# Optimization experiments

Measured on AMD Instinct MI355X. Metric: run time of the kernel, lower is better.

## Reference

```python
import jax, jax.numpy as jnp
import numpy as np

NUM_USERS = 100000
NUM_ITEMS = 100000
EMBED_DIM = 64
BATCH = 4096
MAX_NEIGH = 50


def setup_inputs() -> dict:
    key = jax.random.key(0)
    ks = jax.random.split(key, 12)
    d = EMBED_DIM
    nodes = jax.random.randint(ks[0], (BATCH,), 0, NUM_USERS)
    neighbors = jax.random.randint(ks[1], (BATCH, MAX_NEIGH), 0, NUM_ITEMS)
    lengths = 1 + jax.random.randint(ks[2], (BATCH,), 0, MAX_NEIGH)  # ragged sizes in [1, MAX_NEIGH]
    u_table = jax.random.normal(ks[3], (NUM_USERS, d), dtype=jnp.float32) * 0.1
    i_table = jax.random.normal(ks[4], (NUM_ITEMS, d), dtype=jnp.float32) * 0.1
    # GraphRec-style attention MLP: Linear(2d,d) -> relu -> Linear(d,d) -> relu -> Linear(d,1) -> softmax
    W1 = jax.random.normal(ks[5], (2 * d, d), dtype=jnp.float32) * (1.0 / np.sqrt(2 * d))
    b1 = jnp.zeros((d,), dtype=jnp.float32)
    W2 = jax.random.normal(ks[6], (d, d), dtype=jnp.float32) * (1.0 / np.sqrt(d))
    b2 = jnp.zeros((d,), dtype=jnp.float32)
    W3 = jax.random.normal(ks[7], (d, 1), dtype=jnp.float32) * (1.0 / np.sqrt(d))
    b3 = jnp.zeros((1,), dtype=jnp.float32)
    return {"u_table": u_table, "i_table": i_table, "W1": W1, "b1": b1,
            "W2": W2, "b2": b2, "W3": W3, "b3": b3,
            "nodes": nodes, "neighbors": neighbors, "lengths": lengths}


def reference(u_table, i_table, W1, b1, W2, b2, W3, b3, nodes, neighbors, lengths):
    # is_user=True: gather item features for neighbors, user feature for the node itself.
    neighs = i_table[neighbors]            # [B, L, d]
    node = u_table[nodes]                  # [B, d]
    B, L, d = neighs.shape
    x = jnp.concatenate([neighs, jnp.broadcast_to(node[:, None, :], (B, L, d))], axis=-1)  # [B, L, 2d]
    h = jax.nn.relu(x @ W1 + b1)           # [B, L, d]
    h = jax.nn.relu(h @ W2 + b2)           # [B, L, d]
    logits = (h @ W3 + b3)[..., 0]         # [B, L]
    mask = jnp.arange(L)[None, :] < lengths[:, None]  # ragged neighbor mask
    logits = jnp.where(mask, logits, -jnp.inf)
    att = jax.nn.softmax(logits, axis=1)   # softmax over each node's neighbors (dim=0 per-node in torch)
    # embedding = (neighs^T att)^T  ==  sum_l att[b,l] * neighs[b,l,:]
    return jnp.einsum("bl,bld->bd", att, neighs)  # [B, d]
```

## Files before the change

### kernel.cpp

```cpp
#include <hip/hip_runtime.h>
#include <math.h>

#define LMAX  50
#define NWAVE 2048

typedef short bf16x8 __attribute__((ext_vector_type(8)));
typedef float f32x4  __attribute__((ext_vector_type(4)));
union bfu { bf16x8 v; unsigned u[4]; };

__device__ __forceinline__ unsigned cvt_pk(float lo, float hi) {
    unsigned r;
    asm("v_cvt_pk_bf16_f32 %0, %1, %2" : "=v"(r) : "v"(lo), "v"(hi));
    return r;
}
__device__ __forceinline__ bf16x8 cvt8f(float4 a, float4 b) {
    bfu r;
    r.u[0] = cvt_pk(a.x, a.y); r.u[1] = cvt_pk(a.z, a.w);
    r.u[2] = cvt_pk(b.x, b.y); r.u[3] = cvt_pk(b.z, b.w);
    return r.v;
}
__device__ __forceinline__ float bf2f(short s) {
    union { unsigned u; float f; } v; v.u = ((unsigned)(unsigned short)s) << 16;
    return v.f;
}

__device__ __forceinline__ void process_elem(
    const float* __restrict__ i_table, float* __restrict__ out,
    int b, int len, const int (&idx)[6],
    bf16x8 axu0, bf16x8 axu1,
    const bf16x8 (&w1f)[4][4], const bf16x8 (&w2f)[2][4],
    const float (&b1v)[4], const f32x4 (&b2r)[4], const f32x4 (&w3r)[4],
    unsigned short* __restrict__ hw,
    int l15, int g)
{
    const int g8    = g * 8;
    const int ntile = (len + 15) >> 4;

    float4 LA[2][4];
    #define ISSUE_T(t) if ((t) < ntile) { \
        const float* xp = i_table + (size_t)idx[t] * 64 + g8; \
        LA[(t) & 1][0] = *(const float4*)(xp); \
        LA[(t) & 1][1] = *(const float4*)(xp + 4); \
        LA[(t) & 1][2] = *(const float4*)(xp + 32); \
        LA[(t) & 1][3] = *(const float4*)(xp + 36); \
    }
    ISSUE_T(0)
    ISSUE_T(1)

    f32x4 hn[4];
    #pragma unroll
    for (int nt = 0; nt < 4; ++nt)
        hn[nt] = (f32x4){b1v[nt], b1v[nt], b1v[nt], b1v[nt]};
    #pragma unroll
    for (int nt = 0; nt < 4; ++nt)
        hn[nt] = __builtin_amdgcn_mfma_f32_16x16x32_bf16(axu0, w1f[2][nt], hn[nt], 0, 0, 0);
    #pragma unroll
    for (int nt = 0; nt < 4; ++nt)
        hn[nt] = __builtin_amdgcn_mfma_f32_16x16x32_bf16(axu1, w1f[3][nt], hn[nt], 0, 0, 0);

    float m = -INFINITY, ssum = 0.f;
    float accW[16];
    #pragma unroll
    for (int i = 0; i < 16; ++i) accW[i] = 0.f;

    #pragma unroll
    for (int t = 0; t < 4; ++t) {
        if (t < ntile) {
            bf16x8 a0 = cvt8f(LA[t & 1][0], LA[t & 1][1]);
            bf16x8 a1 = cvt8f(LA[t & 1][2], LA[t & 1][3]);
            if (t + 2 < 4) ISSUE_T(t + 2)

            f32x4 acc[4];
            #pragma unroll
            for (int nt = 0; nt < 4; ++nt) acc[nt] = hn[nt];
            #pragma unroll
            for (int nt = 0; nt < 4; ++nt)
                acc[nt] = __builtin_amdgcn_mfma_f32_16x16x32_bf16(a0, w1f[0][nt], acc[nt], 0, 0, 0);
            #pragma unroll
            for (int nt = 0; nt < 4; ++nt)
                acc[nt] = __builtin_amdgcn_mfma_f32_16x16x32_bf16(a1, w1f[1][nt], acc[nt], 0, 0, 0);

            #pragma unroll
            for (int nt = 0; nt < 4; ++nt) {
                unsigned p0 = cvt_pk(fmaxf(acc[nt][0], 0.f), fmaxf(acc[nt][1], 0.f));
                unsigned p1 = cvt_pk(fmaxf(acc[nt][2], 0.f), fmaxf(acc[nt][3], 0.f));
                hw[(g * 4 + 0) * 72 + nt * 16 + l15] = (unsigned short)p0;
                hw[(g * 4 + 1) * 72 + nt * 16 + l15] = (unsigned short)(p0 >> 16);
                hw[(g * 4 + 2) * 72 + nt * 16 + l15] = (unsigned short)p1;
                hw[(g * 4 + 3) * 72 + nt * 16 + l15] = (unsigned short)(p1 >> 16);
            }
            bf16x8 h0 = *(const bf16x8*)&hw[l15 * 72 + g8];
            bf16x8 h1 = *(const bf16x8*)&hw[l15 * 72 + 32 + g8];

            f32x4 c2[4];
            #pragma unroll
            for (int nt = 0; nt < 4; ++nt) c2[nt] = b2r[nt];
            #pragma unroll
            for (int nt = 0; nt < 4; ++nt)
                c2[nt] = __builtin_amdgcn_mfma_f32_16x16x32_bf16(w2f[0][nt], h0, c2[nt], 0, 0, 0);
            #pragma unroll
            for (int nt = 0; nt < 4; ++nt)
                c2[nt] = __builtin_amdgcn_mfma_f32_16x16x32_bf16(w2f[1][nt], h1, c2[nt], 0, 0, 0);

            float ls = 0.f;
            #pragma unroll
            for (int nt = 0; nt < 4; ++nt) {
                ls = fmaf(fmaxf(c2[nt][0], 0.f), w3r[nt][0], ls);
                ls = fmaf(fmaxf(c2[nt][1], 0.f), w3r[nt][1], ls);
                ls = fmaf(fmaxf(c2[nt][2], 0.f), w3r[nt][2], ls);
                ls = fmaf(fmaxf(c2[nt][3], 0.f), w3r[nt][3], ls);
            }
            ls += __shfl_xor(ls, 16);
            ls += __shfl_xor(ls, 32);

            const int rabs = t * 16 + l15;
            const float lgv = (rabs < len) ? ls : -INFINITY;

            float tm = fmaxf(lgv, __shfl_xor(lgv, 1));
            tm = fmaxf(tm, __shfl_xor(tm, 2));
            tm = fmaxf(tm, __shfl_xor(tm, 4));
            tm = fmaxf(tm, __shfl_xor(tm, 8));
            if (tm > m) {
                const float sc = __expf(m - tm);
                ssum *= sc;
                #pragma unroll
                for (int i = 0; i < 16; ++i) accW[i] *= sc;
                m = tm;
            }
            const float er = __expf(lgv - m);
            ssum += er;

            #pragma unroll
            for (int i = 0; i < 8; ++i) {
                accW[i]     = fmaf(er, bf2f(a0[i]), accW[i]);
                accW[8 + i] = fmaf(er, bf2f(a1[i]), accW[8 + i]);
            }
        }
    }
    #undef ISSUE_T

    #pragma unroll
    for (int i = 0; i < 16; ++i) {
        accW[i] += __shfl_xor(accW[i], 1);
        accW[i] += __shfl_xor(accW[i], 2);
        accW[i] += __shfl_xor(accW[i], 4);
        accW[i] += __shfl_xor(accW[i], 8);
    }
    float ss = ssum;
    ss += __shfl_xor(ss, 1);
    ss += __shfl_xor(ss, 2);
    ss += __shfl_xor(ss, 4);
    ss += __shfl_xor(ss, 8);
    const float inv = 1.f / ss;
    if (l15 == 0) {
        float4 o0 = make_float4(accW[0]  * inv, accW[1]  * inv, accW[2]  * inv, accW[3]  * inv);
        float4 o1 = make_float4(accW[4]  * inv, accW[5]  * inv, accW[6]  * inv, accW[7]  * inv);
        float4 o2 = make_float4(accW[8]  * inv, accW[9]  * inv, accW[10] * inv, accW[11] * inv);
        float4 o3 = make_float4(accW[12] * inv, accW[13] * inv, accW[14] * inv, accW[15] * inv);
        *(float4*)(out + b * 64 +      g8)     = o0;
        *(float4*)(out + b * 64 +      g8 + 4) = o1;
        *(float4*)(out + b * 64 + 32 + g8)     = o2;
        *(float4*)(out + b * 64 + 32 + g8 + 4) = o3;
    }
}

__global__ __launch_bounds__(256, 2) void graphrec_k(
    const float* __restrict__ u_table, const float* __restrict__ i_table,
    const float* __restrict__ W1, const float* __restrict__ b1,
    const float* __restrict__ W2, const float* __restrict__ b2,
    const float* __restrict__ W3, const float* __restrict__ b3,
    const int* __restrict__ nodes, const int* __restrict__ neighbors,
    const int* __restrict__ lengths, float* __restrict__ out)
{
    __shared__ __attribute__((aligned(16))) short WL[24][64][8];
    __shared__ __attribute__((aligned(16))) unsigned short Hs[4][16 * 72];

    const int tid  = threadIdx.x;
    const int w    = tid >> 6, lane = tid & 63;
    const int l15  = lane & 15, g = lane >> 4, g8 = g * 8;

    for (int f = w; f < 24; f += 4) {
        const float* Ws = (f < 16) ? W1 : W2;
        const int    fi = (f < 16) ? f : f - 16;
        const int    ks = fi >> 2, nt = fi & 3;
        const float* p  = Ws + (ks * 32 + g8) * 64 + nt * 16 + l15;
        bfu r;
        r.u[0] = cvt_pk(p[0 * 64], p[1 * 64]);
        r.u[1] = cvt_pk(p[2 * 64], p[3 * 64]);
        r.u[2] = cvt_pk(p[4 * 64], p[5 * 64]);
        r.u[3] = cvt_pk(p[6 * 64], p[7 * 64]);
        *(bf16x8*)&WL[f][lane][0] = r.v;
    }
    __syncthreads();

    bf16x8 w1f[4][4], w2f[2][4];
    #pragma unroll
    for (int ks = 0; ks < 4; ++ks)
        #pragma unroll
        for (int nt = 0; nt < 4; ++nt)
            w1f[ks][nt] = *(const bf16x8*)&WL[ks * 4 + nt][lane][0];
    #pragma unroll
    for (int ks = 0; ks < 2; ++ks)
        #pragma unroll
        for (int nt = 0; nt < 4; ++nt)
            w2f[ks][nt] = *(const bf16x8*)&WL[16 + ks * 4 + nt][lane][0];

    float b1v[4];
    f32x4 b2r[4], w3r[4];
    #pragma unroll
    for (int nt = 0; nt < 4; ++nt) {
        b1v[nt] = b1[nt * 16 + l15];
        b2r[nt] = *(const f32x4*)(b2 + nt * 16 + 4 * g);
        w3r[nt] = *(const f32x4*)(W3 + nt * 16 + 4 * g);
    }

    const int wid = blockIdx.x * 4 + w;
    const int b0  = wid, b1e = wid + NWAVE;

    const int len0 = lengths[b0], len1 = lengths[b1e];
    const int nd0  = nodes[b0],   nd1  = nodes[b1e];

    int idx0[6] = {0, 0, 0, 0, 0, 0}, idx1[6] = {0, 0, 0, 0, 0, 0};
    const int nt0 = (len0 + 15) >> 4, nt1 = (len1 + 15) >> 4;
    #pragma unroll
    for (int t = 0; t < 4; ++t) {
        int r = t * 16 + l15; if (r >= len0) r = len0 - 1;
        if (t < nt0) idx0[t] = neighbors[b0 * LMAX + r];
    }
    #pragma unroll
    for (int t = 0; t < 4; ++t) {
        int r = t * 16 + l15; if (r >= len1) r = len1 - 1;
        if (t < nt1) idx1[t] = neighbors[b1e * LMAX + r];
    }

    const float* up0 = u_table + (size_t)nd0 * 64 + g8;
    const float* up1 = u_table + (size_t)nd1 * 64 + g8;
    float4 U00 = *(const float4*)(up0);
    float4 U01 = *(const float4*)(up0 + 4);
    float4 U02 = *(const float4*)(up0 + 32);
    float4 U03 = *(const float4*)(up0 + 36);
    float4 U10 = *(const float4*)(up1);
    float4 U11 = *(const float4*)(up1 + 4);
    float4 U12 = *(const float4*)(up1 + 32);
    float4 U13 = *(const float4*)(up1 + 36);

    process_elem(i_table, out, b0, len0, idx0,
                 cvt8f(U00, U01), cvt8f(U02, U03),
                 w1f, w2f, b1v, b2r, w3r, &Hs[w][0], l15, g);

    process_elem(i_table, out, b1e, len1, idx1,
                 cvt8f(U10, U11), cvt8f(U12, U13),
                 w1f, w2f, b1v, b2r, w3r, &Hs[w][0], l15, g);
}

extern "C" void kernel_launch(void* const* d_in, const int* in_sizes, int n_in,
                              void* d_out, int out_size, void* d_ws, size_t ws_size,
                              hipStream_t stream) {
    const float* u_table   = (const float*)d_in[0];
    const float* i_table   = (const float*)d_in[1];
    const float* W1        = (const float*)d_in[2];
    const float* b1        = (const float*)d_in[3];
    const float* W2        = (const float*)d_in[4];
    const float* b2        = (const float*)d_in[5];
    const float* W3        = (const float*)d_in[6];
    const float* b3        = (const float*)d_in[7];
    const int*   nodes     = (const int*)d_in[8];
    const int*   neighbors = (const int*)d_in[9];
    const int*   lengths   = (const int*)d_in[10];
    float* out = (float*)d_out;

    graphrec_k<<<dim3(NWAVE / 4), dim3(256), 0, stream>>>(
        u_table, i_table, W1, b1, W2, b2, W3, b3, nodes, neighbors, lengths, out);
}
```

Baseline: 22.41 us.

## Prefetch all neighbor tiles for both batch elements and hoist index loads before weight staging

Moves the lengths, nodes, neighbor index and user-row loads ahead of the shared-memory weight conversion so their latency overlaps with that setup. Instead of a two-deep rolling prefetch per element, all four neighbor tiles of the first element are issued up front, and the second element's tiles are issued interleaved with the first element's compute. This deepens memory-level parallelism for the random gathers but holds 32 float4 registers of staged data per lane, which raises register pressure and may hurt occupancy or cause spills under the 2-block launch bound.

```diff
diff --git a/kernel.cpp b/kernel.cpp
--- a/kernel.cpp
+++ b/kernel.cpp
@@ -24,121 +24,86 @@
     return v.f;
 }
 
-__device__ __forceinline__ void process_elem(
-    const float* __restrict__ i_table, float* __restrict__ out,
-    int b, int len, const int (&idx)[6],
-    bf16x8 axu0, bf16x8 axu1,
+__device__ __forceinline__ void tile_compute(
+    int t, int len, bf16x8 a0, bf16x8 a1,
+    const f32x4 (&hn)[4],
     const bf16x8 (&w1f)[4][4], const bf16x8 (&w2f)[2][4],
-    const float (&b1v)[4], const f32x4 (&b2r)[4], const f32x4 (&w3r)[4],
-    unsigned short* __restrict__ hw,
-    int l15, int g)
+    const f32x4 (&b2r)[4], const f32x4 (&w3r)[4],
+    unsigned short* __restrict__ hw, int l15, int g,
+    float& m, float& ssum, float (&accW)[16])
 {
-    const int g8    = g * 8;
-    const int ntile = (len + 15) >> 4;
-
-    float4 LA[2][4];
-    #define ISSUE_T(t) if ((t) < ntile) { \
-        const float* xp = i_table + (size_t)idx[t] * 64 + g8; \
-        LA[(t) & 1][0] = *(const float4*)(xp); \
-        LA[(t) & 1][1] = *(const float4*)(xp + 4); \
-        LA[(t) & 1][2] = *(const float4*)(xp + 32); \
-        LA[(t) & 1][3] = *(const float4*)(xp + 36); \
-    }
-    ISSUE_T(0)
-    ISSUE_T(1)
-
-    f32x4 hn[4];
-    #pragma unroll
-    for (int nt = 0; nt < 4; ++nt)
-        hn[nt] = (f32x4){b1v[nt], b1v[nt], b1v[nt], b1v[nt]};
-    #pragma unroll
-    for (int nt = 0; nt < 4; ++nt)
-        hn[nt] = __builtin_amdgcn_mfma_f32_16x16x32_bf16(axu0, w1f[2][nt], hn[nt], 0, 0, 0);
-    #pragma unroll
-    for (int nt = 0; nt < 4; ++nt)
-        hn[nt] = __builtin_amdgcn_mfma_f32_16x16x32_bf16(axu1, w1f[3][nt], hn[nt], 0, 0, 0);
-
-    float m = -INFINITY, ssum = 0.f;
-    float accW[16];
-    #pragma unroll
-    for (int i = 0; i < 16; ++i) accW[i] = 0.f;
-
-    #pragma unroll
-    for (int t = 0; t < 4; ++t) {
-        if (t < ntile) {
-            bf16x8 a0 = cvt8f(LA[t & 1][0], LA[t & 1][1]);
-            bf16x8 a1 = cvt8f(LA[t & 1][2], LA[t & 1][3]);
-            if (t + 2 < 4) ISSUE_T(t + 2)
-
-            f32x4 acc[4];
-            #pragma unroll
-            for (int nt = 0; nt < 4; ++nt) acc[nt] = hn[nt];
-            #pragma unroll
-            for (int nt = 0; nt < 4; ++nt)
-                acc[nt] = __builtin_amdgcn_mfma_f32_16x16x32_bf16(a0, w1f[0][nt], acc[nt], 0, 0, 0);
-            #pragma unroll
-            for (int nt = 0; nt < 4; ++nt)
-                acc[nt] = __builtin_amdgcn_mfma_f32_16x16x32_bf16(a1, w1f[1][nt], acc[nt], 0, 0, 0);
-
-            #pragma unroll
-            for (int nt = 0; nt < 4; ++nt) {
-                unsigned p0 = cvt_pk(fmaxf(acc[nt][0], 0.f), fmaxf(acc[nt][1], 0.f));
-                unsigned p1 = cvt_pk(fmaxf(acc[nt][2], 0.f), fmaxf(acc[nt][3], 0.f));
-                hw[(g * 4 + 0) * 72 + nt * 16 + l15] = (unsigned short)p0;
-                hw[(g * 4 + 1) * 72 + nt * 16 + l15] = (unsigned short)(p0 >> 16);
-                hw[(g * 4 + 2) * 72 + nt * 16 + l15] = (unsigned short)p1;
-                hw[(g * 4 + 3) * 72 + nt * 16 + l15] = (unsigned short)(p1 >> 16);
-            }
-            bf16x8 h0 = *(const bf16x8*)&hw[l15 * 72 + g8];
-            bf16x8 h1 = *(const bf16x8*)&hw[l15 * 72 + 32 + g8];
-
-            f32x4 c2[4];
-            #pragma unroll
-            for (int nt = 0; nt < 4; ++nt) c2[nt] = b2r[nt];
-            #pragma unroll
-            for (int nt = 0; nt < 4; ++nt)
-                c2[nt] = __builtin_amdgcn_mfma_f32_16x16x32_bf16(w2f[0][nt], h0, c2[nt], 0, 0, 0);
-            #pragma unroll
-            for (int nt = 0; nt < 4; ++nt)
-                c2[nt] = __builtin_amdgcn_mfma_f32_16x16x32_bf16(w2f[1][nt], h1, c2[nt], 0, 0, 0);
-
-            float ls = 0.f;
-            #pragma unroll
-            for (int nt = 0; nt < 4; ++nt) {
-                ls = fmaf(fmaxf(c2[nt][0], 0.f), w3r[nt][0], ls);
-                ls = fmaf(fmaxf(c2[nt][1], 0.f), w3r[nt][1], ls);
-                ls = fmaf(fmaxf(c2[nt][2], 0.f), w3r[nt][2], ls);
-                ls = fmaf(fmaxf(c2[nt][3], 0.f), w3r[nt][3], ls);
-            }
-            ls += __shfl_xor(ls, 16);
-            ls += __shfl_xor(ls, 32);
-
-            const int rabs = t * 16 + l15;
-            const float lgv = (rabs < len) ? ls : -INFINITY;
-
-            float tm = fmaxf(lgv, __shfl_xor(lgv, 1));
-            tm = fmaxf(tm, __shfl_xor(tm, 2));
-            tm = fmaxf(tm, __shfl_xor(tm, 4));
-            tm = fmaxf(tm, __shfl_xor(tm, 8));
-            if (tm > m) {
-                const float sc = __expf(m - tm);
-                ssum *= sc;
-                #pragma unroll
-                for (int i = 0; i < 16; ++i) accW[i] *= sc;
-                m = tm;
-            }
-            const float er = __expf(lgv - m);
-            ssum += er;
-
-            #pragma unroll
-            for (int i = 0; i < 8; ++i) {
-                accW[i]     = fmaf(er, bf2f(a0[i]), accW[i]);
-                accW[8 + i] = fmaf(er, bf2f(a1[i]), accW[8 + i]);
-            }
-        }
-    }
-    #undef ISSUE_T
-
+    const int g8 = g * 8;
+
+    f32x4 acc[4];
+    #pragma unroll
+    for (int nt = 0; nt < 4; ++nt) acc[nt] = hn[nt];
+    #pragma unroll
+    for (int nt = 0; nt < 4; ++nt)
+        acc[nt] = __builtin_amdgcn_mfma_f32_16x16x32_bf16(a0, w1f[0][nt], acc[nt], 0, 0, 0);
+    #pragma unroll
+    for (int nt = 0; nt < 4; ++nt)
+        acc[nt] = __builtin_amdgcn_mfma_f32_16x16x32_bf16(a1, w1f[1][nt], acc[nt], 0, 0, 0);
+
+    #pragma unroll
+    for (int nt = 0; nt < 4; ++nt) {
+        unsigned p0 = cvt_pk(fmaxf(acc[nt][0], 0.f), fmaxf(acc[nt][1], 0.f));
+        unsigned p1 = cvt_pk(fmaxf(acc[nt][2], 0.f), fmaxf(acc[nt][3], 0.f));
+        hw[(g * 4 + 0) * 72 + nt * 16 + l15] = (unsigned short)p0;
+        hw[(g * 4 + 1) * 72 + nt * 16 + l15] = (unsigned short)(p0 >> 16);
+        hw[(g * 4 + 2) * 72 + nt * 16 + l15] = (unsigned short)p1;
+        hw[(g * 4 + 3) * 72 + nt * 16 + l15] = (unsigned short)(p1 >> 16);
+    }
+    bf16x8 h0 = *(const bf16x8*)&hw[l15 * 72 + g8];
+    bf16x8 h1 = *(const bf16x8*)&hw[l15 * 72 + 32 + g8];
+
+    f32x4 c2[4];
+    #pragma unroll
+    for (int nt = 0; nt < 4; ++nt) c2[nt] = b2r[nt];
+    #pragma unroll
+    for (int nt = 0; nt < 4; ++nt)
+        c2[nt] = __builtin_amdgcn_mfma_f32_16x16x32_bf16(w2f[0][nt], h0, c2[nt], 0, 0, 0);
+    #pragma unroll
+    for (int nt = 0; nt < 4; ++nt)
+        c2[nt] = __builtin_amdgcn_mfma_f32_16x16x32_bf16(w2f[1][nt], h1, c2[nt], 0, 0, 0);
+
+    float ls = 0.f;
+    #pragma unroll
+    for (int nt = 0; nt < 4; ++nt) {
+        ls = fmaf(fmaxf(c2[nt][0], 0.f), w3r[nt][0], ls);
+        ls = fmaf(fmaxf(c2[nt][1], 0.f), w3r[nt][1], ls);
+        ls = fmaf(fmaxf(c2[nt][2], 0.f), w3r[nt][2], ls);
+        ls = fmaf(fmaxf(c2[nt][3], 0.f), w3r[nt][3], ls);
+    }
+    ls += __shfl_xor(ls, 16);
+    ls += __shfl_xor(ls, 32);
+
+    const int rabs = t * 16 + l15;
+    const float lgv = (rabs < len) ? ls : -INFINITY;
+
+    float tm = fmaxf(lgv, __shfl_xor(lgv, 1));
+    tm = fmaxf(tm, __shfl_xor(tm, 2));
+    tm = fmaxf(tm, __shfl_xor(tm, 4));
+    tm = fmaxf(tm, __shfl_xor(tm, 8));
+    if (tm > m) {
+        const float sc = __expf(m - tm);
+        ssum *= sc;
+        #pragma unroll
+        for (int i = 0; i < 16; ++i) accW[i] *= sc;
+        m = tm;
+    }
+    const float er = __expf(lgv - m);
+    ssum += er;
+    #pragma unroll
+    for (int i = 0; i < 8; ++i) {
+        accW[i]     = fmaf(er, bf2f(a0[i]), accW[i]);
+        accW[8 + i] = fmaf(er, bf2f(a1[i]), accW[8 + i]);
+    }
+}
+
+__device__ __forceinline__ void finalize_elem(
+    float (&accW)[16], float ssum, float* __restrict__ out,
+    int b, int l15, int g)
+{
     #pragma unroll
     for (int i = 0; i < 16; ++i) {
         accW[i] += __shfl_xor(accW[i], 1);
@@ -152,6 +117,7 @@
     ss += __shfl_xor(ss, 4);
     ss += __shfl_xor(ss, 8);
     const float inv = 1.f / ss;
+    const int g8 = g * 8;
     if (l15 == 0) {
         float4 o0 = make_float4(accW[0]  * inv, accW[1]  * inv, accW[2]  * inv, accW[3]  * inv);
         float4 o1 = make_float4(accW[4]  * inv, accW[5]  * inv, accW[6]  * inv, accW[7]  * inv);
@@ -178,6 +144,31 @@
     const int tid  = threadIdx.x;
     const int w    = tid >> 6, lane = tid & 63;
     const int l15  = lane & 15, g = lane >> 4, g8 = g * 8;
+
+    const int wid = blockIdx.x * 4 + w;
+    const int b0  = wid, b1e = wid + NWAVE;
+    const int len0 = lengths[b0], len1 = lengths[b1e];
+    const int nd0  = nodes[b0],   nd1  = nodes[b1e];
+    const int nt0  = (len0 + 15) >> 4, nt1 = (len1 + 15) >> 4;
+
+    int idx0[4], idx1[4];
+    #pragma unroll
+    for (int t = 0; t < 4; ++t) {
+        int r0 = t * 16 + l15; if (r0 >= len0) r0 = len0 - 1;
+        idx0[t] = (t < nt0) ? neighbors[b0 * LMAX + r0] : 0;
+        int r1 = t * 16 + l15; if (r1 >= len1) r1 = len1 - 1;
+        idx1[t] = (t < nt1) ? neighbors[b1e * LMAX + r1] : 0;
+    }
+    const float* up0 = u_table + (size_t)nd0 * 64 + g8;
+    const float* up1 = u_table + (size_t)nd1 * 64 + g8;
+    float4 U00 = *(const float4*)(up0);
+    float4 U01 = *(const float4*)(up0 + 4);
+    float4 U02 = *(const float4*)(up0 + 32);
+    float4 U03 = *(const float4*)(up0 + 36);
+    float4 U10 = *(const float4*)(up1);
+    float4 U11 = *(const float4*)(up1 + 4);
+    float4 U12 = *(const float4*)(up1 + 32);
+    float4 U13 = *(const float4*)(up1 + 36);
 
     for (int f = w; f < 24; f += 4) {
         const float* Ws = (f < 16) ? W1 : W2;
@@ -214,52 +205,94 @@
         w3r[nt] = *(const f32x4*)(W3 + nt * 16 + 4 * g);
     }
 
-    const int wid = blockIdx.x * 4 + w;
-    const int b0  = wid, b1e = wid + NWAVE;
-
-    const int len0 = lengths[b0], len1 = lengths[b1e];
-    const int nd0  = nodes[b0],   nd1  = nodes[b1e];
-
-    int idx0[6] = {0, 0, 0, 0, 0, 0}, idx1[6] = {0, 0, 0, 0, 0, 0};
-    const int nt0 = (len0 + 15) >> 4, nt1 = (len1 + 15) >> 4;
+    float4 LA0[4][4], LA1[4][4];
+    #define ISSUE0(t) if ((t) < nt0) { \
+        const float* xp = i_table + (size_t)idx0[t] * 64 + g8; \
+        LA0[t][0] = *(const float4*)(xp); \
+        LA0[t][1] = *(const float4*)(xp + 4); \
+        LA0[t][2] = *(const float4*)(xp + 32); \
+        LA0[t][3] = *(const float4*)(xp + 36); \
+    }
+    #define ISSUE1(t) if ((t) < nt1) { \
+        const float* xp = i_table + (size_t)idx1[t] * 64 + g8; \
+        LA1[t][0] = *(const float4*)(xp); \
+        LA1[t][1] = *(const float4*)(xp + 4); \
+        LA1[t][2] = *(const float4*)(xp + 32); \
+        LA1[t][3] = *(const float4*)(xp + 36); \
+    }
+    ISSUE0(0) ISSUE0(1) ISSUE0(2) ISSUE0(3)
+
+    bf16x8 ax0 = cvt8f(U00, U01), ax1 = cvt8f(U02, U03);
+    f32x4 hn0[4];
+    #pragma unroll
+    for (int nt = 0; nt < 4; ++nt)
+        hn0[nt] = (f32x4){b1v[nt], b1v[nt], b1v[nt], b1v[nt]};
+    #pragma unroll
+    for (int nt = 0; nt < 4; ++nt)
+        hn0[nt] = __builtin_amdgcn_mfma_f32_16x16x32_bf16(ax0, w1f[2][nt], hn0[nt], 0, 0, 0);
+    #pragma unroll
+    for (int nt = 0; nt < 4; ++nt)
+        hn0[nt] = __builtin_amdgcn_mfma_f32_16x16x32_bf16(ax1, w1f[3][nt], hn0[nt], 0, 0, 0);
+
+    unsigned short* hw = &Hs[w][0];
+
+    float m0 = -INFINITY, ss0 = 0.f;
+    float accW0[16];
+    #pragma unroll
+    for (int i = 0; i < 16; ++i) accW0[i] = 0.f;
+
     #pragma unroll
     for (int t = 0; t < 4; ++t) {
-        int r = t * 16 + l15; if (r >= len0) r = len0 - 1;
-        if (t < nt0) idx0[t] = neighbors[b0 * LMAX + r];
-    }
+        if (t < nt0) {
+            bf16x8 a0 = cvt8f(LA0[t][0], LA0[t][1]);
+            bf16x8 a1 = cvt8f(LA0[t][2], LA0[t][3]);
+            ISSUE1(t)
+            tile_compute(t, len0, a0, a1, hn0, w1f, w2f, b2r, w3r,
+                         hw, l15, g, m0, ss0, accW0);
+        } else {
+            ISSUE1(t)
+        }
+    }
+    finalize_elem(accW0, ss0, out, b0, l15, g);
+
+    bf16x8 bx0 = cvt8f(U10, U11), bx1 = cvt8f(U12, U13);
+    f32x4 hn1[4];
+    #pragma unroll
+    for (int nt = 0; nt < 4; ++nt)
+        hn1[nt] = (f32x4){b1v[nt], b1v[nt], b1v[nt], b1v[nt]};
+    #pragma unroll
+    for (int nt = 0; nt < 4; ++nt)
+        hn1[nt] = __builtin_amdgcn_mfma_f32_16x16x32_bf16(bx0, w1f[2][nt], hn1[nt], 0, 0, 0);
+    #pragma unroll
+    for (int nt = 0; nt < 4; ++nt)
+        hn1[nt] = __builtin_amdgcn_mfma_f32_16x16x32_bf16(bx1, w1f[3][nt], hn1[nt], 0, 0, 0);
+
+    float m1 = -INFINITY, ss1 = 0.f;
+    float accW1[16];
+    #pragma unroll
+    for (int i = 0; i < 16; ++i) accW1[i] = 0.f;
+
     #pragma unroll
     for (int t = 0; t < 4; ++t) {
-        int r = t * 16 + l15; if (r >= len1) r = len1 - 1;
-        if (t < nt1) idx1[t] = neighbors[b1e * LMAX + r];
-    }
-
-    const float* up0 = u_table + (size_t)nd0 * 64 + g8;
-    const float* up1 = u_table + (size_t)nd1 * 64 + g8;
-    float4 U00 = *(const float4*)(up0);
-    float4 U01 = *(const float4*)(up0 + 4);
-    float4 U02 = *(const float4*)(up0 + 32);
-    float4 U03 = *(const float4*)(up0 + 36);
-    float4 U10 = *(const float4*)(up1);
-    float4 U11 = *(const float4*)(up1 + 4);
-    float4 U12 = *(const float4*)(up1 + 32);
-    float4 U13 = *(const float4*)(up1 + 36);
-
-    process_elem(i_table, out, b0, len0, idx0,
-                 cvt8f(U00, U01), cvt8f(U02, U03),
-                 w1f, w2f, b1v, b2r, w3r, &Hs[w][0], l15, g);
-
-    process_elem(i_table, out, b1e, len1, idx1,
-                 cvt8f(U10, U11), cvt8f(U12, U13),
-                 w1f, w2f, b1v, b2r, w3r, &Hs[w][0], l15, g);
+        if (t < nt1) {
+            bf16x8 a0 = cvt8f(LA1[t][0], LA1[t][1]);
+            bf16x8 a1 = cvt8f(LA1[t][2], LA1[t][3]);
+            tile_compute(t, len1, a0, a1, hn1, w1f, w2f, b2r, w3r,
+                         hw, l15, g, m1, ss1, accW1);
+        }
+    }
+    finalize_elem(accW1, ss1, out, b1e, l15, g);
+    #undef ISSUE0
+    #undef ISSUE1
 }
 
 extern "C" void kernel_launch(void* const* d_in, const int* in_sizes, int n_in,
                               void* d_out, int out_size, void* d_ws, size_t ws_size,
                               hipStream_t stream) {
     const float* u_table   = (const float*)d_in[0];
+    const float* b1        = (const float*)d_in[3];
     const float* i_table   = (const float*)d_in[1];
     const float* W1        = (const float*)d_in[2];
-    const float* b1        = (const float*)d_in[3];
     const float* W2        = (const float*)d_in[4];
     const float* b2        = (const float*)d_in[5];
     const float* W3        = (const float*)d_in[6];
```

Result: slower. 30.81 us (+37.5%).

## Process neighbor tiles in pairs to interleave independent MFMA chains

Applied to the files above, without the earlier changes.

Restructures the per-node tile loop so two 16-row neighbor tiles are handled together: both layer-1 MFMA chains are issued back to back, both hidden tiles go through separate LDS buffers, and the online-softmax max/rescale happens once per pair. It also prefetches tiles 2 and 3 right after the first pair is converted instead of a rolling double buffer. The goal is to expose more independent MFMA work to hide dependency latency and halve the softmax reduction steps. In exchange it uses more registers (four load buffers, two accumulator sets) and doubles per-wave LDS scratch, which may pressure occupancy at launch_bounds(256,2).

```diff
diff --git a/kernel.cpp b/kernel.cpp
--- a/kernel.cpp
+++ b/kernel.cpp
@@ -24,25 +24,155 @@
     return v.f;
 }
 
+__device__ __forceinline__ void pair_compute(
+    int t0, int len, bool vB,
+    bf16x8 a0A, bf16x8 a1A, bf16x8 a0B, bf16x8 a1B,
+    const f32x4 (&hn)[4],
+    const bf16x8 (&w1f)[4][4], const bf16x8 (&w2f)[2][4],
+    const f32x4 (&b2r)[4], const f32x4 (&w3r)[4],
+    unsigned short* __restrict__ hw, int l15, int g,
+    float& m, float& ssum, float (&accW)[16])
+{
+    const int g8 = g * 8;
+    unsigned short* hwA = hw;
+    unsigned short* hwB = hw + 16 * 72;
+
+    f32x4 accA[4], accB[4];
+    #pragma unroll
+    for (int nt = 0; nt < 4; ++nt) { accA[nt] = hn[nt]; accB[nt] = hn[nt]; }
+    #pragma unroll
+    for (int nt = 0; nt < 4; ++nt)
+        accA[nt] = __builtin_amdgcn_mfma_f32_16x16x32_bf16(a0A, w1f[0][nt], accA[nt], 0, 0, 0);
+    #pragma unroll
+    for (int nt = 0; nt < 4; ++nt)
+        accA[nt] = __builtin_amdgcn_mfma_f32_16x16x32_bf16(a1A, w1f[1][nt], accA[nt], 0, 0, 0);
+    if (vB) {
+        #pragma unroll
+        for (int nt = 0; nt < 4; ++nt)
+            accB[nt] = __builtin_amdgcn_mfma_f32_16x16x32_bf16(a0B, w1f[0][nt], accB[nt], 0, 0, 0);
+        #pragma unroll
+        for (int nt = 0; nt < 4; ++nt)
+            accB[nt] = __builtin_amdgcn_mfma_f32_16x16x32_bf16(a1B, w1f[1][nt], accB[nt], 0, 0, 0);
+    }
+
+    #pragma unroll
+    for (int nt = 0; nt < 4; ++nt) {
+        unsigned p0 = cvt_pk(fmaxf(accA[nt][0], 0.f), fmaxf(accA[nt][1], 0.f));
+        unsigned p1 = cvt_pk(fmaxf(accA[nt][2], 0.f), fmaxf(accA[nt][3], 0.f));
+        hwA[(g * 4 + 0) * 72 + nt * 16 + l15] = (unsigned short)p0;
+        hwA[(g * 4 + 1) * 72 + nt * 16 + l15] = (unsigned short)(p0 >> 16);
+        hwA[(g * 4 + 2) * 72 + nt * 16 + l15] = (unsigned short)p1;
+        hwA[(g * 4 + 3) * 72 + nt * 16 + l15] = (unsigned short)(p1 >> 16);
+    }
+    if (vB) {
+        #pragma unroll
+        for (int nt = 0; nt < 4; ++nt) {
+            unsigned p0 = cvt_pk(fmaxf(accB[nt][0], 0.f), fmaxf(accB[nt][1], 0.f));
+            unsigned p1 = cvt_pk(fmaxf(accB[nt][2], 0.f), fmaxf(accB[nt][3], 0.f));
+            hwB[(g * 4 + 0) * 72 + nt * 16 + l15] = (unsigned short)p0;
+            hwB[(g * 4 + 1) * 72 + nt * 16 + l15] = (unsigned short)(p0 >> 16);
+            hwB[(g * 4 + 2) * 72 + nt * 16 + l15] = (unsigned short)p1;
+            hwB[(g * 4 + 3) * 72 + nt * 16 + l15] = (unsigned short)(p1 >> 16);
+        }
+    }
+    bf16x8 h0A = *(const bf16x8*)&hwA[l15 * 72 + g8];
+    bf16x8 h1A = *(const bf16x8*)&hwA[l15 * 72 + 32 + g8];
+
+    f32x4 c2A[4], c2B[4];
+    #pragma unroll
+    for (int nt = 0; nt < 4; ++nt) c2A[nt] = b2r[nt];
+    #pragma unroll
+    for (int nt = 0; nt < 4; ++nt)
+        c2A[nt] = __builtin_amdgcn_mfma_f32_16x16x32_bf16(w2f[0][nt], h0A, c2A[nt], 0, 0, 0);
+    #pragma unroll
+    for (int nt = 0; nt < 4; ++nt)
+        c2A[nt] = __builtin_amdgcn_mfma_f32_16x16x32_bf16(w2f[1][nt], h1A, c2A[nt], 0, 0, 0);
+    if (vB) {
+        bf16x8 h0B = *(const bf16x8*)&hwB[l15 * 72 + g8];
+        bf16x8 h1B = *(const bf16x8*)&hwB[l15 * 72 + 32 + g8];
+        #pragma unroll
+        for (int nt = 0; nt < 4; ++nt) c2B[nt] = b2r[nt];
+        #pragma unroll
+        for (int nt = 0; nt < 4; ++nt)
+            c2B[nt] = __builtin_amdgcn_mfma_f32_16x16x32_bf16(w2f[0][nt], h0B, c2B[nt], 0, 0, 0);
+        #pragma unroll
+        for (int nt = 0; nt < 4; ++nt)
+            c2B[nt] = __builtin_amdgcn_mfma_f32_16x16x32_bf16(w2f[1][nt], h1B, c2B[nt], 0, 0, 0);
+    }
+
+    float lsA = 0.f, lsB = 0.f;
+    #pragma unroll
+    for (int nt = 0; nt < 4; ++nt) {
+        lsA = fmaf(fmaxf(c2A[nt][0], 0.f), w3r[nt][0], lsA);
+        lsA = fmaf(fmaxf(c2A[nt][1], 0.f), w3r[nt][1], lsA);
+        lsA = fmaf(fmaxf(c2A[nt][2], 0.f), w3r[nt][2], lsA);
+        lsA = fmaf(fmaxf(c2A[nt][3], 0.f), w3r[nt][3], lsA);
+    }
+    lsA += __shfl_xor(lsA, 16);
+    lsA += __shfl_xor(lsA, 32);
+    if (vB) {
+        #pragma unroll
+        for (int nt = 0; nt < 4; ++nt) {
+            lsB = fmaf(fmaxf(c2B[nt][0], 0.f), w3r[nt][0], lsB);
+            lsB = fmaf(fmaxf(c2B[nt][1], 0.f), w3r[nt][1], lsB);
+            lsB = fmaf(fmaxf(c2B[nt][2], 0.f), w3r[nt][2], lsB);
+            lsB = fmaf(fmaxf(c2B[nt][3], 0.f), w3r[nt][3], lsB);
+        }
+        lsB += __shfl_xor(lsB, 16);
+        lsB += __shfl_xor(lsB, 32);
+    }
+
+    const float lgvA = (t0 * 16 + l15 < len) ? lsA : -INFINITY;
+    const float lgvB = vB ? (((t0 + 1) * 16 + l15 < len) ? lsB : -INFINITY) : -INFINITY;
+
+    float pm = fmaxf(lgvA, lgvB);
+    pm = fmaxf(pm, __shfl_xor(pm, 1));
+    pm = fmaxf(pm, __shfl_xor(pm, 2));
+    pm = fmaxf(pm, __shfl_xor(pm, 4));
+    pm = fmaxf(pm, __shfl_xor(pm, 8));
+    if (pm > m) {
+        const float sc = __expf(m - pm);
+        ssum *= sc;
+        #pragma unroll
+        for (int i = 0; i < 16; ++i) accW[i] *= sc;
+        m = pm;
+    }
+    const float erA = __expf(lgvA - m);
+    ssum += erA;
+    #pragma unroll
+    for (int i = 0; i < 8; ++i) {
+        accW[i]     = fmaf(erA, bf2f(a0A[i]), accW[i]);
+        accW[8 + i] = fmaf(erA, bf2f(a1A[i]), accW[8 + i]);
+    }
+    if (vB) {
+        const float erB = __expf(lgvB - m);
+        ssum += erB;
+        #pragma unroll
+        for (int i = 0; i < 8; ++i) {
+            accW[i]     = fmaf(erB, bf2f(a0B[i]), accW[i]);
+            accW[8 + i] = fmaf(erB, bf2f(a1B[i]), accW[8 + i]);
+        }
+    }
+}
+
 __device__ __forceinline__ void process_elem(
     const float* __restrict__ i_table, float* __restrict__ out,
-    int b, int len, const int (&idx)[6],
+    int b, int len, const int (&idx)[4],
     bf16x8 axu0, bf16x8 axu1,
     const bf16x8 (&w1f)[4][4], const bf16x8 (&w2f)[2][4],
     const float (&b1v)[4], const f32x4 (&b2r)[4], const f32x4 (&w3r)[4],
-    unsigned short* __restrict__ hw,
-    int l15, int g)
+    unsigned short* __restrict__ hw, int l15, int g)
 {
     const int g8    = g * 8;
     const int ntile = (len + 15) >> 4;
 
-    float4 LA[2][4];
+    float4 LA[4][4];
     #define ISSUE_T(t) if ((t) < ntile) { \
         const float* xp = i_table + (size_t)idx[t] * 64 + g8; \
-        LA[(t) & 1][0] = *(const float4*)(xp); \
-        LA[(t) & 1][1] = *(const float4*)(xp + 4); \
-        LA[(t) & 1][2] = *(const float4*)(xp + 32); \
-        LA[(t) & 1][3] = *(const float4*)(xp + 36); \
+        LA[t][0] = *(const float4*)(xp); \
+        LA[t][1] = *(const float4*)(xp + 4); \
+        LA[t][2] = *(const float4*)(xp + 32); \
+        LA[t][3] = *(const float4*)(xp + 36); \
     }
     ISSUE_T(0)
     ISSUE_T(1)
@@ -63,79 +193,29 @@
     #pragma unroll
     for (int i = 0; i < 16; ++i) accW[i] = 0.f;
 
-    #pragma unroll
-    for (int t = 0; t < 4; ++t) {
-        if (t < ntile) {
-            bf16x8 a0 = cvt8f(LA[t & 1][0], LA[t & 1][1]);
-            bf16x8 a1 = cvt8f(LA[t & 1][2], LA[t & 1][3]);
-            if (t + 2 < 4) ISSUE_T(t + 2)
-
-            f32x4 acc[4];
-            #pragma unroll
-            for (int nt = 0; nt < 4; ++nt) acc[nt] = hn[nt];
-            #pragma unroll
-            for (int nt = 0; nt < 4; ++nt)
-                acc[nt] = __builtin_amdgcn_mfma_f32_16x16x32_bf16(a0, w1f[0][nt], acc[nt], 0, 0, 0);
-            #pragma unroll
-            for (int nt = 0; nt < 4; ++nt)
-                acc[nt] = __builtin_amdgcn_mfma_f32_16x16x32_bf16(a1, w1f[1][nt], acc[nt], 0, 0, 0);
-
-            #pragma unroll
-            for (int nt = 0; nt < 4; ++nt) {
-                unsigned p0 = cvt_pk(fmaxf(acc[nt][0], 0.f), fmaxf(acc[nt][1], 0.f));
-                unsigned p1 = cvt_pk(fmaxf(acc[nt][2], 0.f), fmaxf(acc[nt][3], 0.f));
-                hw[(g * 4 + 0) * 72 + nt * 16 + l15] = (unsigned short)p0;
-                hw[(g * 4 + 1) * 72 + nt * 16 + l15] = (unsigned short)(p0 >> 16);
-                hw[(g * 4 + 2) * 72 + nt * 16 + l15] = (unsigned short)p1;
-                hw[(g * 4 + 3) * 72 + nt * 16 + l15] = (unsigned short)(p1 >> 16);
-            }
-            bf16x8 h0 = *(const bf16x8*)&hw[l15 * 72 + g8];
-            bf16x8 h1 = *(const bf16x8*)&hw[l15 * 72 + 32 + g8];
-
-            f32x4 c2[4];
-            #pragma unroll
-            for (int nt = 0; nt < 4; ++nt) c2[nt] = b2r[nt];
-            #pragma unroll
-            for (int nt = 0; nt < 4; ++nt)
-                c2[nt] = __builtin_amdgcn_mfma_f32_16x16x32_bf16(w2f[0][nt], h0, c2[nt], 0, 0, 0);
-            #pragma unroll
-            for (int nt = 0; nt < 4; ++nt)
-                c2[nt] = __builtin_amdgcn_mfma_f32_16x16x32_bf16(w2f[1][nt], h1, c2[nt], 0, 0, 0);
-
-            float ls = 0.f;
-            #pragma unroll
-            for (int nt = 0; nt < 4; ++nt) {
-                ls = fmaf(fmaxf(c2[nt][0], 0.f), w3r[nt][0], ls);
-                ls = fmaf(fmaxf(c2[nt][1], 0.f), w3r[nt][1], ls);
-                ls = fmaf(fmaxf(c2[nt][2], 0.f), w3r[nt][2], ls);
-                ls = fmaf(fmaxf(c2[nt][3], 0.f), w3r[nt][3], ls);
-            }
-            ls += __shfl_xor(ls, 16);
-            ls += __shfl_xor(ls, 32);
-
-            const int rabs = t * 16 + l15;
-            const float lgv = (rabs < len) ? ls : -INFINITY;
-
-            float tm = fmaxf(lgv, __shfl_xor(lgv, 1));
-            tm = fmaxf(tm, __shfl_xor(tm, 2));
-            tm = fmaxf(tm, __shfl_xor(tm, 4));
-            tm = fmaxf(tm, __shfl_xor(tm, 8));
-            if (tm > m) {
-                const float sc = __expf(m - tm);
-                ssum *= sc;
-                #pragma unroll
-                for (int i = 0; i < 16; ++i) accW[i] *= sc;
-                m = tm;
-            }
-            const float er = __expf(lgv - m);
-            ssum += er;
-
-            #pragma unroll
-            for (int i = 0; i < 8; ++i) {
-                accW[i]     = fmaf(er, bf2f(a0[i]), accW[i]);
-                accW[8 + i] = fmaf(er, bf2f(a1[i]), accW[8 + i]);
-            }
-        }
+    {
+        bf16x8 a0A = cvt8f(LA[0][0], LA[0][1]);
+        bf16x8 a1A = cvt8f(LA[0][2], LA[0][3]);
+        bf16x8 a0B = {0,0,0,0,0,0,0,0}, a1B = {0,0,0,0,0,0,0,0};
+        if (ntile > 1) {
+            a0B = cvt8f(LA[1][0], LA[1][1]);
+            a1B = cvt8f(LA[1][2], LA[1][3]);
+        }
+        ISSUE_T(2)
+        ISSUE_T(3)
+        pair_compute(0, len, ntile > 1, a0A, a1A, a0B, a1B,
+                     hn, w1f, w2f, b2r, w3r, hw, l15, g, m, ssum, accW);
+    }
+    if (ntile > 2) {
+        bf16x8 a0A = cvt8f(LA[2][0], LA[2][1]);
+        bf16x8 a1A = cvt8f(LA[2][2], LA[2][3]);
+        bf16x8 a0B = {0,0,0,0,0,0,0,0}, a1B = {0,0,0,0,0,0,0,0};
+        if (ntile > 3) {
+            a0B = cvt8f(LA[3][0], LA[3][1]);
+            a1B = cvt8f(LA[3][2], LA[3][3]);
+        }
+        pair_compute(2, len, ntile > 3, a0A, a1A, a0B, a1B,
+                     hn, w1f, w2f, b2r, w3r, hw, l15, g, m, ssum, accW);
     }
     #undef ISSUE_T
 
@@ -173,7 +253,7 @@
     const int* __restrict__ lengths, float* __restrict__ out)
 {
     __shared__ __attribute__((aligned(16))) short WL[24][64][8];
-    __shared__ __attribute__((aligned(16))) unsigned short Hs[4][16 * 72];
+    __shared__ __attribute__((aligned(16))) unsigned short Hs[4][2 * 16 * 72];
 
     const int tid  = threadIdx.x;
     const int w    = tid >> 6, lane = tid & 63;
@@ -220,17 +300,17 @@
     const int len0 = lengths[b0], len1 = lengths[b1e];
     const int nd0  = nodes[b0],   nd1  = nodes[b1e];
 
-    int idx0[6] = {0, 0, 0, 0, 0, 0}, idx1[6] = {0, 0, 0, 0, 0, 0};
+    int idx0[4], idx1[4];
     const int nt0 = (len0 + 15) >> 4, nt1 = (len1 + 15) >> 4;
     #pragma unroll
     for (int t = 0; t < 4; ++t) {
         int r = t * 16 + l15; if (r >= len0) r = len0 - 1;
-        if (t < nt0) idx0[t] = neighbors[b0 * LMAX + r];
+        idx0[t] = (t < nt0) ? neighbors[b0 * LMAX + r] : 0;
     }
     #pragma unroll
     for (int t = 0; t < 4; ++t) {
         int r = t * 16 + l15; if (r >= len1) r = len1 - 1;
-        if (t < nt1) idx1[t] = neighbors[b1e * LMAX + r];
+        idx1[t] = (t < nt1) ? neighbors[b1e * LMAX + r] : 0;
     }
 
     const float* up0 = u_table + (size_t)nd0 * 64 + g8;
```

New measurement: 26.64 us. 18.9% more time.
